# Kernel tuning notes

Measured on AMD Instinct MI355X. Metric: run time of the kernel, lower is better.

## Reference

```python
import jax, jax.numpy as jnp
import numpy as np

D_MODEL = 512
NUM_HEADS = 8
D_K = D_MODEL // NUM_HEADS


def setup_inputs() -> dict:
    key = jax.random.key(0)
    ks = jax.random.split(key, 9)
    B, N = 4, 2048
    x = jax.random.normal(ks[0], (B, N, D_MODEL), dtype=jnp.float32)
    s = 1.0 / np.sqrt(D_MODEL)
    Wq = jax.random.normal(ks[1], (D_MODEL, D_MODEL), dtype=jnp.float32) * s
    bq = jax.random.normal(ks[2], (D_MODEL,), dtype=jnp.float32) * 0.02
    Wk = jax.random.normal(ks[3], (D_MODEL, D_MODEL), dtype=jnp.float32) * s
    bk = jax.random.normal(ks[4], (D_MODEL,), dtype=jnp.float32) * 0.02
    Wv = jax.random.normal(ks[5], (D_MODEL, D_MODEL), dtype=jnp.float32) * s
    bv = jax.random.normal(ks[6], (D_MODEL,), dtype=jnp.float32) * 0.02
    Wo = jax.random.normal(ks[7], (D_MODEL, D_MODEL), dtype=jnp.float32) * s
    bo = jax.random.normal(ks[8], (D_MODEL,), dtype=jnp.float32) * 0.02
    return {"x": x, "Wq": Wq, "bq": bq, "Wk": Wk, "bk": bk,
            "Wv": Wv, "bv": bv, "Wo": Wo, "bo": bo}


def reference(x, Wq, bq, Wk, bk, Wv, bv, Wo, bo):
    B, N, _ = x.shape
    # project and split heads: [B, H, N, d_k]
    def split_heads(t):
        return t.reshape(B, N, NUM_HEADS, D_K).transpose(0, 2, 1, 3)
    Q = split_heads(x @ Wq + bq)
    K = split_heads(x @ Wk + bk)
    V = split_heads(x @ Wv + bv)
    scale = 1.0 / np.sqrt(D_K)
    scores = jnp.einsum('bhqd,bhkd->bhqk', Q, K) * scale  # [B,H,N,N]
    probs = jax.nn.softmax(scores, axis=-1)
    attn = jnp.einsum('bhqk,bhkd->bhqd', probs, V)
    attn = attn.transpose(0, 2, 1, 3).reshape(B, N, D_MODEL)
    return attn @ Wo + bo
```

## Files before the change

### kernel.cpp

```cpp
#include <hip/hip_runtime.h>
#include <math.h>

#define D_MODEL 512
#define N_SEQ   2048
#define H       8
#define DK      64

typedef __attribute__((ext_vector_type(8)))  short bf16x8;
typedef __attribute__((ext_vector_type(4)))  float f32x4;
typedef __attribute__((ext_vector_type(16))) float f32x16;

__device__ __forceinline__ unsigned short f2b(float f) {
    unsigned int u = __float_as_uint(f);
    u += 0x7FFF + ((u >> 16) & 1);
    return (unsigned short)(u >> 16);
}

__device__ __forceinline__ unsigned int pack2(float lo, float hi) {
#if __has_builtin(__builtin_amdgcn_cvt_pk_bf16_f32)
    typedef __attribute__((ext_vector_type(2))) short bf16x2;
    bf16x2 p = __builtin_amdgcn_cvt_pk_bf16_f32(lo, hi);
    return (unsigned int)(unsigned short)p[0] |
           ((unsigned int)(unsigned short)p[1] << 16);
#else
    return (unsigned int)f2b(lo) | ((unsigned int)f2b(hi) << 16);
#endif
}

__device__ __forceinline__ float fexp2(float x) {
#if __has_builtin(__builtin_amdgcn_exp2f)
    return __builtin_amdgcn_exp2f(x);
#else
    return __expf(x * 0.6931471805599453f);
#endif
}

#define SC2 0.18033688011112042f

__global__ void convert_bf16(const float* __restrict__ in,
                             unsigned short* __restrict__ out)
{
    const int i = (blockIdx.x * 256 + threadIdx.x) * 8;
    float4 a = *(const float4*)(in + i);
    float4 b = *(const float4*)(in + i + 4);
    unsigned int w[4];
    w[0] = pack2(a.x, a.y); w[1] = pack2(a.z, a.w);
    w[2] = pack2(b.x, b.y); w[3] = pack2(b.z, b.w);
    *(bf16x8*)(out + i) = *(bf16x8*)w;
}

__global__ void transpose_all(
    const float* __restrict__ W0, const float* __restrict__ W1,
    const float* __restrict__ W2, const float* __restrict__ W3,
    unsigned short* __restrict__ T0, unsigned short* __restrict__ T1,
    unsigned short* __restrict__ T2, unsigned short* __restrict__ T3)
{
    const float* W; unsigned short* Wt;
    if      (blockIdx.z == 0) { W = W0; Wt = T0; }
    else if (blockIdx.z == 1) { W = W1; Wt = T1; }
    else if (blockIdx.z == 2) { W = W2; Wt = T2; }
    else                      { W = W3; Wt = T3; }

    __shared__ float t[32][33];
    const int tx = threadIdx.x, ty = threadIdx.y;
    const int x = blockIdx.x * 32 + tx;
    const int y0 = blockIdx.y * 32;
    for (int i = ty; i < 32; i += 8)
        t[i][tx] = W[(size_t)(y0 + i) * D_MODEL + x];
    __syncthreads();
    const int ox = blockIdx.y * 32 + tx;
    const int oy0 = blockIdx.x * 32;
    for (int i = ty; i < 32; i += 8)
        Wt[(size_t)(oy0 + i) * D_MODEL + ox] = f2b(t[tx][i]);
}

__global__ __launch_bounds__(256, 4) void gemm_qkv(
    const unsigned short* __restrict__ xb,
    const unsigned short* __restrict__ Wtq,
    const unsigned short* __restrict__ Wtk,
    const unsigned short* __restrict__ Wtv,
    const float* __restrict__ bq, const float* __restrict__ bk,
    const float* __restrict__ bv,
    unsigned short* __restrict__ Qb, unsigned short* __restrict__ Kb,
    unsigned short* __restrict__ Vtb)
{
    __shared__ unsigned short As[128][72];
    __shared__ unsigned short Bs[64][72];

    const unsigned short* Wt; const float* bias; unsigned short* out; int isV;
    float sc;
    if (blockIdx.z == 0)      { Wt = Wtq; bias = bq; out = Qb;  isV = 0; sc = SC2; }
    else if (blockIdx.z == 1) { Wt = Wtk; bias = bk; out = Kb;  isV = 0; sc = 1.0f; }
    else                      { Wt = Wtv; bias = bv; out = Vtb; isV = 1; sc = 1.0f; }

    const int tid  = threadIdx.x;
    const int lane = tid & 63, wave = tid >> 6;
    const int m0 = blockIdx.y * 128, n0 = blockIdx.x * 64;
    const int wm = (wave & 1) * 64, wn = (wave >> 1) * 32;
    const int cn = lane & 15, g = lane >> 4;

    const int arow = tid >> 1, acol = (tid & 1) * 32;
    const int brow = tid >> 2, bcol = (tid & 3) * 16;
    const unsigned short* Ag = xb + (size_t)(m0 + arow) * D_MODEL + acol;
    const unsigned short* Bg = Wt + (size_t)(n0 + brow) * D_MODEL + bcol;

    f32x4 acc[4][2];
    #pragma unroll
    for (int i = 0; i < 4; ++i)
        #pragma unroll
        for (int j = 0; j < 2; ++j)
            acc[i][j] = (f32x4){0.f, 0.f, 0.f, 0.f};

    for (int k0 = 0; k0 < D_MODEL; k0 += 64) {
        bf16x8 av[4], bv2[2];
        #pragma unroll
        for (int q = 0; q < 4; ++q) av[q] = *(const bf16x8*)(Ag + k0 + q * 8);
        #pragma unroll
        for (int q = 0; q < 2; ++q) bv2[q] = *(const bf16x8*)(Bg + k0 + q * 8);
        __syncthreads();
        #pragma unroll
        for (int q = 0; q < 4; ++q) *(bf16x8*)&As[arow][acol + q * 8] = av[q];
        #pragma unroll
        for (int q = 0; q < 2; ++q) *(bf16x8*)&Bs[brow][bcol + q * 8] = bv2[q];
        __syncthreads();

        #pragma unroll
        for (int ks = 0; ks < 2; ++ks) {
            bf16x8 af[4], bf[2];
            #pragma unroll
            for (int i = 0; i < 4; ++i)
                af[i] = *(const bf16x8*)&As[wm + i * 16 + cn][ks * 32 + g * 8];
            #pragma unroll
            for (int j = 0; j < 2; ++j)
                bf[j] = *(const bf16x8*)&Bs[wn + j * 16 + cn][ks * 32 + g * 8];
            if (!isV) {
                #pragma unroll
                for (int i = 0; i < 4; ++i)
                    #pragma unroll
                    for (int j = 0; j < 2; ++j)
                        acc[i][j] = __builtin_amdgcn_mfma_f32_16x16x32_bf16(
                            bf[j], af[i], acc[i][j], 0, 0, 0);
            } else {
                #pragma unroll
                for (int i = 0; i < 4; ++i)
                    #pragma unroll
                    for (int j = 0; j < 2; ++j)
                        acc[i][j] = __builtin_amdgcn_mfma_f32_16x16x32_bf16(
                            af[i], bf[j], acc[i][j], 0, 0, 0);
            }
        }
    }

    if (!isV) {
        #pragma unroll
        for (int j = 0; j < 2; ++j) {
            const int dbase = n0 + wn + j * 16 + g * 4;
            const int hh = dbase >> 6, dd = dbase & 63;
            float4 bb = *(const float4*)&bias[dbase];
            #pragma unroll
            for (int i = 0; i < 4; ++i) {
                const int tt = m0 + wm + i * 16 + cn;
                const int bi = tt >> 11, tok = tt & (N_SEQ - 1);
                ushort4 pk;
                pk.x = f2b((acc[i][j][0] + bb.x) * sc);
                pk.y = f2b((acc[i][j][1] + bb.y) * sc);
                pk.z = f2b((acc[i][j][2] + bb.z) * sc);
                pk.w = f2b((acc[i][j][3] + bb.w) * sc);
                *(ushort4*)(out + (((size_t)bi * H + hh) * N_SEQ + tok) * DK + dd) = pk;
            }
        }
    } else {
        #pragma unroll
        for (int j = 0; j < 2; ++j) {
            const int n = n0 + wn + j * 16 + cn;
            const int hh = n >> 6, dd = n & 63;
            const float bb = bias[n];
            #pragma unroll
            for (int i = 0; i < 4; ++i) {
                const int m = m0 + wm + i * 16 + g * 4;
                const int bi = m >> 11, t = m & (N_SEQ - 1);
                ushort4 pk;
                pk.x = f2b(acc[i][j][0] + bb);
                pk.y = f2b(acc[i][j][1] + bb);
                pk.z = f2b(acc[i][j][2] + bb);
                pk.w = f2b(acc[i][j][3] + bb);
                *(ushort4*)(out + (((size_t)bi * H + hh) * DK + dd) * N_SEQ + t) = pk;
            }
        }
    }
}

__global__ __launch_bounds__(256, 4) void gemm_o(
    const unsigned short* __restrict__ A,
    const unsigned short* __restrict__ Wt,
    const float* __restrict__ bias, float* __restrict__ out)
{
    __shared__ unsigned short As[64][72];
    __shared__ unsigned short Bs[64][72];

    const int tid  = threadIdx.x;
    const int lane = tid & 63, wave = tid >> 6;
    const int m0 = blockIdx.y * 64, n0 = blockIdx.x * 64;
    const int wm = (wave & 1) * 32, wn = (wave >> 1) * 32;
    const int cn = lane & 15, g = lane >> 4;

    const int srow = tid >> 2;
    const int scol = (tid & 3) * 16;
    const unsigned short* Ag = A  + (size_t)(m0 + srow) * D_MODEL + scol;
    const unsigned short* Bg = Wt + (size_t)(n0 + srow) * D_MODEL + scol;

    f32x4 acc[2][2];
    #pragma unroll
    for (int i = 0; i < 2; ++i)
        #pragma unroll
        for (int j = 0; j < 2; ++j)
            acc[i][j] = (f32x4){0.f, 0.f, 0.f, 0.f};

    for (int k0 = 0; k0 < D_MODEL; k0 += 64) {
        bf16x8 av[2], bv[2];
        #pragma unroll
        for (int q = 0; q < 2; ++q) {
            av[q] = *(const bf16x8*)(Ag + k0 + q * 8);
            bv[q] = *(const bf16x8*)(Bg + k0 + q * 8);
        }
        __syncthreads();
        #pragma unroll
        for (int q = 0; q < 2; ++q) {
            *(bf16x8*)&As[srow][scol + q * 8] = av[q];
            *(bf16x8*)&Bs[srow][scol + q * 8] = bv[q];
        }
        __syncthreads();

        #pragma unroll
        for (int ks = 0; ks < 2; ++ks) {
            bf16x8 af[2], bf[2];
            #pragma unroll
            for (int i = 0; i < 2; ++i)
                af[i] = *(const bf16x8*)&As[wm + i * 16 + cn][ks * 32 + g * 8];
            #pragma unroll
            for (int j = 0; j < 2; ++j)
                bf[j] = *(const bf16x8*)&Bs[wn + j * 16 + cn][ks * 32 + g * 8];
            #pragma unroll
            for (int i = 0; i < 2; ++i)
                #pragma unroll
                for (int j = 0; j < 2; ++j)
                    acc[i][j] = __builtin_amdgcn_mfma_f32_16x16x32_bf16(
                        af[i], bf[j], acc[i][j], 0, 0, 0);
        }
    }

    #pragma unroll
    for (int j = 0; j < 2; ++j) {
        const int n = n0 + wn + j * 16 + cn;
        const float bb = bias[n];
        #pragma unroll
        for (int i = 0; i < 2; ++i)
            #pragma unroll
            for (int r = 0; r < 4; ++r) {
                const int m = m0 + wm + i * 16 + g * 4 + r;
                out[(size_t)m * D_MODEL + n] = acc[i][j][r] + bb;
            }
    }
}

__global__ __launch_bounds__(256, 4) void attn_mfma(
    const unsigned short* __restrict__ Q,
    const unsigned short* __restrict__ K,
    const unsigned short* __restrict__ Vt,
    unsigned short* __restrict__ ctx)
{
    __shared__ unsigned short SM[2][2][64][72];

    const int bid = blockIdx.x;
    const int qt = (bid >> 3) & 31;
    const int bh = (bid & 7) * 4 + (bid >> 8);
    const int b = bh >> 3, h = bh & 7;

    const int tid = threadIdx.x, lane = tid & 63, wave = tid >> 6;
    const int sp = wave >> 1;
    const int w4 = wave & 1;
    const int lq = lane & 31, hf = lane >> 5;
    const int qs = qt * 64 + w4 * 32;

    const size_t hb = (size_t)b * H + h;
    const unsigned short* Qp = Q  + hb * N_SEQ * DK;
    const unsigned short* Kp = K  + hb * N_SEQ * DK;
    const unsigned short* Vp = Vt + hb * DK * N_SEQ;

    bf16x8 qf[4];
    #pragma unroll
    for (int kd = 0; kd < 4; ++kd)
        qf[kd] = *(const bf16x8*)(Qp + (size_t)(qs + lq) * DK + kd * 16 + hf * 8);

    f32x16 O[2], Ol;
    #pragma unroll
    for (int r = 0; r < 16; ++r) { O[0][r] = 0.f; O[1][r] = 0.f; Ol[r] = 0.f; }

    bf16x8 onesA;
    {
        const short v = (lq == 0) ? (short)0x3F80 : (short)0;
        #pragma unroll
        for (int j = 0; j < 8; ++j) onesA[j] = v;
    }

    const int sps = tid >> 7;
    const int tl = tid & 127;
    const int krow = tl >> 1, kcol = (tl & 1) * 32;
    unsigned short (*Kss)[72] = SM[sps][0];
    unsigned short (*Vss)[72] = SM[sps][1];
    unsigned short (*Ks)[72]  = SM[sp][0];
    unsigned short (*Vs)[72]  = SM[sp][1];

    for (int it = 0; it < 16; ++it) {
        const int j0 = sps * (N_SEQ / 2) + it * 64;
        bf16x8 kv[4], vv[4];
        #pragma unroll
        for (int q = 0; q < 4; ++q) {
            kv[q] = *(const bf16x8*)(Kp + (size_t)(j0 + krow) * DK + kcol + q * 8);
            vv[q] = *(const bf16x8*)(Vp + (size_t)krow * N_SEQ + j0 + kcol + q * 8);
        }
        bf16x8 sw[4];
        {
            ushort4* v0 = (ushort4*)&vv[0]; ushort4* v1 = (ushort4*)&vv[1];
            ushort4* v2 = (ushort4*)&vv[2]; ushort4* v3 = (ushort4*)&vv[3];
            ushort4* s0 = (ushort4*)&sw[0]; ushort4* s1 = (ushort4*)&sw[1];
            ushort4* s2 = (ushort4*)&sw[2]; ushort4* s3 = (ushort4*)&sw[3];
            s0[0] = v0[0]; s0[1] = v1[0];
            s1[0] = v0[1]; s1[1] = v1[1];
            s2[0] = v2[0]; s2[1] = v3[0];
            s3[0] = v2[1]; s3[1] = v3[1];
        }
        __syncthreads();
        #pragma unroll
        for (int q = 0; q < 4; ++q) {
            *(bf16x8*)&Kss[krow][kcol + q * 8] = kv[q];
            *(bf16x8*)&Vss[krow][kcol + q * 8] = sw[q];
        }
        __syncthreads();

        f32x16 s0, s1;
        #pragma unroll
        for (int r = 0; r < 16; ++r) { s0[r] = 0.f; s1[r] = 0.f; }
        #pragma unroll
        for (int kd = 0; kd < 4; ++kd) {
            bf16x8 a0 = *(const bf16x8*)&Ks[lq][kd * 16 + hf * 8];
            bf16x8 a1 = *(const bf16x8*)&Ks[32 + lq][kd * 16 + hf * 8];
            s0 = __builtin_amdgcn_mfma_f32_32x32x16_bf16(a0, qf[kd], s0, 0, 0, 0);
            s1 = __builtin_amdgcn_mfma_f32_32x32x16_bf16(a1, qf[kd], s1, 0, 0, 0);
        }

        unsigned int pk0[4][2], pk1[4][2];
        #pragma unroll
        for (int c = 0; c < 4; ++c)
            #pragma unroll
            for (int p = 0; p < 2; ++p) {
                pk0[c][p] = pack2(fexp2(s0[4 * c + 2 * p]),
                                  fexp2(s0[4 * c + 2 * p + 1]));
                pk1[c][p] = pack2(fexp2(s1[4 * c + 2 * p]),
                                  fexp2(s1[4 * c + 2 * p + 1]));
            }

        #pragma unroll
        for (int ks = 0; ks < 4; ++ks) {
            const unsigned int (*src)[2] = (ks < 2) ? pk0 : pk1;
            const int c2 = (ks & 1) * 2;
            bf16x8 bp;
            unsigned int* bpu = (unsigned int*)&bp;
            bpu[0] = src[c2][0];     bpu[1] = src[c2][1];
            bpu[2] = src[c2 + 1][0]; bpu[3] = src[c2 + 1][1];
            bf16x8 va0 = *(const bf16x8*)&Vs[lq][ks * 16 + hf * 8];
            bf16x8 va1 = *(const bf16x8*)&Vs[32 + lq][ks * 16 + hf * 8];
            O[0] = __builtin_amdgcn_mfma_f32_32x32x16_bf16(va0, bp, O[0], 0, 0, 0);
            O[1] = __builtin_amdgcn_mfma_f32_32x32x16_bf16(va1, bp, O[1], 0, 0, 0);
            Ol   = __builtin_amdgcn_mfma_f32_32x32x16_bf16(onesA, bp, Ol, 0, 0, 0);
        }
    }

    float* R    = (float*)&SM[0][0][0][0];
    float* Laux = R + 2 * 64 * 32;

    __syncthreads();
    if (sp == 1) {
        #pragma unroll
        for (int dt = 0; dt < 2; ++dt)
            #pragma unroll
            for (int r = 0; r < 16; ++r) {
                const int d = (r & 3) + 8 * (r >> 2) + 4 * hf + 32 * dt;
                R[(w4 * 64 + d) * 32 + lq] = O[dt][r];
            }
        if (hf == 0) Laux[w4 * 32 + lq] = Ol[0];
    }
    __syncthreads();
    if (sp == 0) {
        #pragma unroll
        for (int dt = 0; dt < 2; ++dt)
            #pragma unroll
            for (int r = 0; r < 16; ++r) {
                const int d = (r & 3) + 8 * (r >> 2) + 4 * hf + 32 * dt;
                O[dt][r] += R[(w4 * 64 + d) * 32 + lq];
            }
        const float lsum = Ol[0] + Laux[w4 * 32 + lq];
        const float linv = 1.0f / __shfl(lsum, lq);

        unsigned short* ob = ctx + ((size_t)b * N_SEQ + qs + lq) * D_MODEL
                                 + h * DK + hf * 4;
        #pragma unroll
        for (int dt = 0; dt < 2; ++dt)
            #pragma unroll
            for (int c = 0; c < 4; ++c) {
                unsigned int w2[2];
                w2[0] = pack2(O[dt][4 * c + 0] * linv, O[dt][4 * c + 1] * linv);
                w2[1] = pack2(O[dt][4 * c + 2] * linv, O[dt][4 * c + 3] * linv);
                *(unsigned int*)(ob + dt * 32 + c * 8)     = w2[0];
                *(unsigned int*)(ob + dt * 32 + c * 8 + 2) = w2[1];
            }
    }
}

extern "C" void kernel_launch(void* const* d_in, const int* in_sizes, int n_in,
                              void* d_out, int out_size, void* d_ws, size_t ws_size,
                              hipStream_t stream)
{
    const float* x  = (const float*)d_in[0];
    const float* Wq = (const float*)d_in[1];
    const float* bq = (const float*)d_in[2];
    const float* Wk = (const float*)d_in[3];
    const float* bk = (const float*)d_in[4];
    const float* Wv = (const float*)d_in[5];
    const float* bv = (const float*)d_in[6];
    const float* Wo = (const float*)d_in[7];
    const float* bo = (const float*)d_in[8];
    float* out = (float*)d_out;

    const int M = in_sizes[0] / D_MODEL;
    const size_t NX = (size_t)M * D_MODEL;
    const size_t NW = (size_t)D_MODEL * D_MODEL;

    unsigned short* xb  = (unsigned short*)d_ws;
    unsigned short* Wtq = xb + NX;
    unsigned short* Wtk = Wtq + NW;
    unsigned short* Wtv = Wtk + NW;
    unsigned short* Wto = Wtv + NW;
    unsigned short* Qb  = Wto + NW;
    unsigned short* Kb  = Qb + NX;
    unsigned short* Vtb = Kb + NX;
    unsigned short* ctx = Vtb + NX;

    convert_bf16<<<NX / (256 * 8), 256, 0, stream>>>(x, xb);
    transpose_all<<<dim3(16, 16, 4), dim3(32, 8), 0, stream>>>(
        Wq, Wk, Wv, Wo, Wtq, Wtk, Wtv, Wto);

    gemm_qkv<<<dim3(D_MODEL / 64, M / 128, 3), 256, 0, stream>>>(
        xb, Wtq, Wtk, Wtv, bq, bk, bv, Qb, Kb, Vtb);
    attn_mfma<<<1024, 256, 0, stream>>>(Qb, Kb, Vtb, ctx);
    gemm_o<<<dim3(D_MODEL / 64, M / 64), 256, 0, stream>>>(ctx, Wto, bo, out);
}
```

Baseline: 185.5 us.

## Process two 32-row query subtiles per wave to reuse K/V fragments

Each wave in the attention kernel now handles 64 query rows (two 32-row subtiles) instead of 32. The K and V fragments are loaded from shared memory once per key tile and reused for both subtiles, so the grid halves to 512 blocks and K/V global loads per query drop by half. The cost is roughly doubled accumulator and register use, with launch bounds relaxed to 2 blocks per SM, which lowers occupancy. With 512 blocks on a 256-CU part, the tail balance also changes.

```diff
diff --git a/kernel.cpp b/kernel.cpp
--- a/kernel.cpp
+++ b/kernel.cpp
@@ -263,7 +263,7 @@
     }
 }
 
-__global__ __launch_bounds__(256, 4) void attn_mfma(
+__global__ __launch_bounds__(256, 2) void attn_mfma(
     const unsigned short* __restrict__ Q,
     const unsigned short* __restrict__ K,
     const unsigned short* __restrict__ Vt,
@@ -272,29 +272,36 @@
     __shared__ unsigned short SM[2][2][64][72];
 
     const int bid = blockIdx.x;
-    const int qt = (bid >> 3) & 31;
-    const int bh = (bid & 7) * 4 + (bid >> 8);
+    const int qt = (bid >> 3) & 15;
+    const int bh = (bid & 7) * 4 + (bid >> 7);
     const int b = bh >> 3, h = bh & 7;
 
     const int tid = threadIdx.x, lane = tid & 63, wave = tid >> 6;
     const int sp = wave >> 1;
     const int w4 = wave & 1;
     const int lq = lane & 31, hf = lane >> 5;
-    const int qs = qt * 64 + w4 * 32;
+    const int qbase = qt * 128 + w4 * 64;
 
     const size_t hb = (size_t)b * H + h;
     const unsigned short* Qp = Q  + hb * N_SEQ * DK;
     const unsigned short* Kp = K  + hb * N_SEQ * DK;
     const unsigned short* Vp = Vt + hb * DK * N_SEQ;
 
-    bf16x8 qf[4];
+    bf16x8 qf[2][4];
     #pragma unroll
-    for (int kd = 0; kd < 4; ++kd)
-        qf[kd] = *(const bf16x8*)(Qp + (size_t)(qs + lq) * DK + kd * 16 + hf * 8);
-
-    f32x16 O[2], Ol;
+    for (int u = 0; u < 2; ++u)
+        #pragma unroll
+        for (int kd = 0; kd < 4; ++kd)
+            qf[u][kd] = *(const bf16x8*)(Qp +
+                (size_t)(qbase + u * 32 + lq) * DK + kd * 16 + hf * 8);
+
+    f32x16 O[2][2], Ol[2];
     #pragma unroll
-    for (int r = 0; r < 16; ++r) { O[0][r] = 0.f; O[1][r] = 0.f; Ol[r] = 0.f; }
+    for (int u = 0; u < 2; ++u)
+        #pragma unroll
+        for (int r = 0; r < 16; ++r) {
+            O[u][0][r] = 0.f; O[u][1][r] = 0.f; Ol[u][r] = 0.f;
+        }
 
     bf16x8 onesA;
     {
@@ -338,82 +345,105 @@
         }
         __syncthreads();
 
-        f32x16 s0, s1;
-        #pragma unroll
-        for (int r = 0; r < 16; ++r) { s0[r] = 0.f; s1[r] = 0.f; }
+        bf16x8 ka0[4], ka1[4];
         #pragma unroll
         for (int kd = 0; kd < 4; ++kd) {
-            bf16x8 a0 = *(const bf16x8*)&Ks[lq][kd * 16 + hf * 8];
-            bf16x8 a1 = *(const bf16x8*)&Ks[32 + lq][kd * 16 + hf * 8];
-            s0 = __builtin_amdgcn_mfma_f32_32x32x16_bf16(a0, qf[kd], s0, 0, 0, 0);
-            s1 = __builtin_amdgcn_mfma_f32_32x32x16_bf16(a1, qf[kd], s1, 0, 0, 0);
-        }
-
-        unsigned int pk0[4][2], pk1[4][2];
-        #pragma unroll
-        for (int c = 0; c < 4; ++c)
-            #pragma unroll
-            for (int p = 0; p < 2; ++p) {
-                pk0[c][p] = pack2(fexp2(s0[4 * c + 2 * p]),
-                                  fexp2(s0[4 * c + 2 * p + 1]));
-                pk1[c][p] = pack2(fexp2(s1[4 * c + 2 * p]),
-                                  fexp2(s1[4 * c + 2 * p + 1]));
-            }
-
+            ka0[kd] = *(const bf16x8*)&Ks[lq][kd * 16 + hf * 8];
+            ka1[kd] = *(const bf16x8*)&Ks[32 + lq][kd * 16 + hf * 8];
+        }
+
+        unsigned int pA[2][4][2], pB[2][4][2];
+        #pragma unroll
+        for (int u = 0; u < 2; ++u) {
+            f32x16 s0, s1;
+            #pragma unroll
+            for (int r = 0; r < 16; ++r) { s0[r] = 0.f; s1[r] = 0.f; }
+            #pragma unroll
+            for (int kd = 0; kd < 4; ++kd) {
+                s0 = __builtin_amdgcn_mfma_f32_32x32x16_bf16(ka0[kd], qf[u][kd], s0, 0, 0, 0);
+                s1 = __builtin_amdgcn_mfma_f32_32x32x16_bf16(ka1[kd], qf[u][kd], s1, 0, 0, 0);
+            }
+            #pragma unroll
+            for (int c = 0; c < 4; ++c)
+                #pragma unroll
+                for (int p = 0; p < 2; ++p) {
+                    pA[u][c][p] = pack2(fexp2(s0[4 * c + 2 * p]),
+                                        fexp2(s0[4 * c + 2 * p + 1]));
+                    pB[u][c][p] = pack2(fexp2(s1[4 * c + 2 * p]),
+                                        fexp2(s1[4 * c + 2 * p + 1]));
+                }
+        }
+
+        bf16x8 va0[4], va1[4];
         #pragma unroll
         for (int ks = 0; ks < 4; ++ks) {
-            const unsigned int (*src)[2] = (ks < 2) ? pk0 : pk1;
-            const int c2 = (ks & 1) * 2;
-            bf16x8 bp;
-            unsigned int* bpu = (unsigned int*)&bp;
-            bpu[0] = src[c2][0];     bpu[1] = src[c2][1];
-            bpu[2] = src[c2 + 1][0]; bpu[3] = src[c2 + 1][1];
-            bf16x8 va0 = *(const bf16x8*)&Vs[lq][ks * 16 + hf * 8];
-            bf16x8 va1 = *(const bf16x8*)&Vs[32 + lq][ks * 16 + hf * 8];
-            O[0] = __builtin_amdgcn_mfma_f32_32x32x16_bf16(va0, bp, O[0], 0, 0, 0);
-            O[1] = __builtin_amdgcn_mfma_f32_32x32x16_bf16(va1, bp, O[1], 0, 0, 0);
-            Ol   = __builtin_amdgcn_mfma_f32_32x32x16_bf16(onesA, bp, Ol, 0, 0, 0);
-        }
+            va0[ks] = *(const bf16x8*)&Vs[lq][ks * 16 + hf * 8];
+            va1[ks] = *(const bf16x8*)&Vs[32 + lq][ks * 16 + hf * 8];
+        }
+
+        #pragma unroll
+        for (int u = 0; u < 2; ++u)
+            #pragma unroll
+            for (int ks = 0; ks < 4; ++ks) {
+                const unsigned int (*src)[2] = (ks < 2) ? pA[u] : pB[u];
+                const int c2 = (ks & 1) * 2;
+                bf16x8 bp;
+                unsigned int* bpu = (unsigned int*)&bp;
+                bpu[0] = src[c2][0];     bpu[1] = src[c2][1];
+                bpu[2] = src[c2 + 1][0]; bpu[3] = src[c2 + 1][1];
+                O[u][0] = __builtin_amdgcn_mfma_f32_32x32x16_bf16(va0[ks], bp, O[u][0], 0, 0, 0);
+                O[u][1] = __builtin_amdgcn_mfma_f32_32x32x16_bf16(va1[ks], bp, O[u][1], 0, 0, 0);
+                Ol[u]   = __builtin_amdgcn_mfma_f32_32x32x16_bf16(onesA,   bp, Ol[u],   0, 0, 0);
+            }
     }
 
     float* R    = (float*)&SM[0][0][0][0];
-    float* Laux = R + 2 * 64 * 32;
+    float* Laux = R + 2 * 2 * 64 * 32;
 
     __syncthreads();
     if (sp == 1) {
         #pragma unroll
-        for (int dt = 0; dt < 2; ++dt)
-            #pragma unroll
-            for (int r = 0; r < 16; ++r) {
-                const int d = (r & 3) + 8 * (r >> 2) + 4 * hf + 32 * dt;
-                R[(w4 * 64 + d) * 32 + lq] = O[dt][r];
-            }
-        if (hf == 0) Laux[w4 * 32 + lq] = Ol[0];
+        for (int u = 0; u < 2; ++u) {
+            #pragma unroll
+            for (int dt = 0; dt < 2; ++dt)
+                #pragma unroll
+                for (int r = 0; r < 16; ++r) {
+                    const int d = (r & 3) + 8 * (r >> 2) + 4 * hf + 32 * dt;
+                    R[(((w4 * 2 + u) * 64) + d) * 32 + lq] = O[u][dt][r];
+                }
+            if (hf == 0) Laux[(w4 * 2 + u) * 32 + lq] = Ol[u][0];
+        }
     }
     __syncthreads();
     if (sp == 0) {
         #pragma unroll
-        for (int dt = 0; dt < 2; ++dt)
-            #pragma unroll
-            for (int r = 0; r < 16; ++r) {
-                const int d = (r & 3) + 8 * (r >> 2) + 4 * hf + 32 * dt;
-                O[dt][r] += R[(w4 * 64 + d) * 32 + lq];
-            }
-        const float lsum = Ol[0] + Laux[w4 * 32 + lq];
-        const float linv = 1.0f / __shfl(lsum, lq);
-
-        unsigned short* ob = ctx + ((size_t)b * N_SEQ + qs + lq) * D_MODEL
-                                 + h * DK + hf * 4;
-        #pragma unroll
-        for (int dt = 0; dt < 2; ++dt)
-            #pragma unroll
-            for (int c = 0; c < 4; ++c) {
-                unsigned int w2[2];
-                w2[0] = pack2(O[dt][4 * c + 0] * linv, O[dt][4 * c + 1] * linv);
-                w2[1] = pack2(O[dt][4 * c + 2] * linv, O[dt][4 * c + 3] * linv);
-                *(unsigned int*)(ob + dt * 32 + c * 8)     = w2[0];
-                *(unsigned int*)(ob + dt * 32 + c * 8 + 2) = w2[1];
-            }
+        for (int u = 0; u < 2; ++u) {
+            #pragma unroll
+            for (int dt = 0; dt < 2; ++dt)
+                #pragma unroll
+                for (int r = 0; r < 16; ++r) {
+                    const int d = (r & 3) + 8 * (r >> 2) + 4 * hf + 32 * dt;
+                    O[u][dt][r] += R[(((w4 * 2 + u) * 64) + d) * 32 + lq];
+                }
+            const float lsum = Ol[u][0] + Laux[(w4 * 2 + u) * 32 + lq];
+            const float linv = 1.0f / __shfl(lsum, lq);
+
+            unsigned short* ob = ctx +
+                ((size_t)b * N_SEQ + qbase + u * 32 + lq) * D_MODEL
+                + h * DK + hf * 4;
+            #pragma unroll
+            for (int dt = 0; dt < 2; ++dt)
+                #pragma unroll
+                for (int c = 0; c < 4; ++c) {
+                    unsigned int w2[2];
+                    w2[0] = pack2(O[u][dt][4 * c + 0] * linv,
+                                  O[u][dt][4 * c + 1] * linv);
+                    w2[1] = pack2(O[u][dt][4 * c + 2] * linv,
+                                  O[u][dt][4 * c + 3] * linv);
+                    *(unsigned int*)(ob + dt * 32 + c * 8)     = w2[0];
+                    *(unsigned int*)(ob + dt * 32 + c * 8 + 2) = w2[1];
+                }
+        }
     }
 }
 
@@ -452,6 +482,6 @@
 
     gemm_qkv<<<dim3(D_MODEL / 64, M / 128, 3), 256, 0, stream>>>(
         xb, Wtq, Wtk, Wtv, bq, bk, bv, Qb, Kb, Vtb);
-    attn_mfma<<<1024, 256, 0, stream>>>(Qb, Kb, Vtb, ctx);
+    attn_mfma<<<512, 256, 0, stream>>>(Qb, Kb, Vtb, ctx);
     gemm_o<<<dim3(D_MODEL / 64, M / 64), 256, 0, stream>>>(ctx, Wto, bo, out);
 }
```

After: 179.1 us. -3.5%, faster.
